# Kernel optimization log

Hardware: AMD Instinct MI355X
Metric: run time of the kernel (lower is better)

## Reference

```python
import jax, jax.numpy as jnp
import numpy as np
from jax import lax

EPS = 1e-5


def maxpool3x3(x):
    # 3x3 max pool, stride 1, pad 1 (NCHW)
    return lax.reduce_window(x, -jnp.inf, lax.max,
                             window_dimensions=(1, 1, 3, 3),
                             window_strides=(1, 1, 1, 1),
                             padding=((0, 0), (0, 0), (1, 1), (1, 1)))


def focus_downsample(x):
    B, C, H, W = x.shape
    pad_h = (3 - H % 3) % 3
    pad_w = (3 - W % 3) % 3
    if pad_h or pad_w:
        x = jnp.pad(x, ((0, 0), (0, 0), (0, pad_h), (0, pad_w)))
    return jnp.concatenate([x[..., i::3, j::3] for i in range(3) for j in range(3)], axis=1)


def batchnorm(x, gamma, beta):
    # training-mode BatchNorm2d: stats over (B,H,W)
    mean = jnp.mean(x, axis=(0, 2, 3), keepdims=True)
    var = jnp.var(x, axis=(0, 2, 3), keepdims=True)
    g = gamma.reshape(1, -1, 1, 1)
    b = beta.reshape(1, -1, 1, 1)
    return (x - mean) * jax.lax.rsqrt(var + EPS) * g + b


def dwconv(x, w, pad_h, pad_w):
    # depthwise conv, w: (C,1,kh,kw)
    return lax.conv_general_dilated(x, w, window_strides=(1, 1),
                                    padding=((pad_h, pad_h), (pad_w, pad_w)),
                                    dimension_numbers=('NCHW', 'OIHW', 'NCHW'),
                                    feature_group_count=x.shape[1])


def h_transform(x):
    B, C, H, W = x.shape
    x = jnp.pad(x, ((0, 0), (0, 0), (0, 0), (0, W)))
    x = x.reshape(B, C, -1)[..., :-W]
    return x.reshape(B, C, H, 2 * W - 1)


def inv_h_transform(x):
    B, C, H, _ = x.shape
    x = x.reshape(B, C, -1)
    x = jnp.pad(x, ((0, 0), (0, 0), (0, H)))
    x = x.reshape(B, C, H, 2 * H)
    return x[..., :H]


def v_transform(x):
    return h_transform(x.transpose(0, 1, 3, 2)).transpose(0, 1, 3, 2)


def inv_v_transform(x):
    return inv_h_transform(x.transpose(0, 1, 3, 2)).transpose(0, 1, 3, 2)


def pixel_shuffle3(x):
    B, C9, h, w = x.shape
    C = C9 // 9
    x = x.reshape(B, C, 3, 3, h, w)
    x = x.transpose(0, 1, 4, 2, 5, 3)  # B,C,h,3,w,3
    return x.reshape(B, C, 3 * h, 3 * w)


def setup_inputs() -> dict:
    key = jax.random.key(0)
    ks = jax.random.split(key, 10)
    C, K = 64, 11
    B, H, W = 16, 144, 144
    s = 0.05
    return {
        'x': jax.random.normal(ks[0], (B, C, H, W), jnp.float32),
        'w_mixer': jax.random.normal(ks[1], (9, C, C), jnp.float32) * s,
        'g_mnorm': jnp.ones((9 * C,), jnp.float32),
        'b_mnorm': jnp.zeros((9 * C,), jnp.float32),
        'w_h1': jax.random.normal(ks[2], (C, 1, K, 3), jnp.float32) * s,
        'w_v1': jax.random.normal(ks[3], (C, 1, 3, K), jnp.float32) * s,
        'w_h2': jax.random.normal(ks[4], (C, 1, K, 3), jnp.float32) * s,
        'w_v2': jax.random.normal(ks[5], (C, 1, 3, K), jnp.float32) * s,
        'g_norm': jnp.ones((C,), jnp.float32),
        'b_norm': jnp.zeros((C,), jnp.float32),
    }


def reference(x, w_mixer, g_mnorm, b_mnorm, w_h1, w_v1, w_h2, w_v2, g_norm, b_norm):
    C = w_h1.shape[0]
    K = w_h1.shape[2]
    pad = K // 2
    H, W = x.shape[-2:]

    x_pool = maxpool3x3(x)
    x_focus = focus_downsample(x_pool)               # (B,9C,H/3,W/3)

    # grouped 1x1 conv, groups=9
    B, _, h, w = x_focus.shape
    xg = x_focus.reshape(B, 9, C, h, w)
    x_mixed = jnp.einsum('goi,bgihw->bgohw', w_mixer, xg).reshape(B, 9 * C, h, w)
    x_mixed = batchnorm(x_mixed, g_mnorm, b_mnorm)

    x_tem, x_key = x_mixed[:, :C], x_mixed[:, C:]

    x_h1 = dwconv(x_tem, w_h1, pad, 1)
    x_w1 = dwconv(x_tem, w_v1, 1, pad)
    x_h2 = inv_h_transform(dwconv(h_transform(x_tem), w_h2, pad, 1))
    x_w2 = inv_v_transform(dwconv(v_transform(x_tem), w_v2, 1, pad))

    att_map = batchnorm(x_h1 + x_w1 + x_h2 + x_w2, g_norm, b_norm)
    final_features = jnp.concatenate([att_map, x_key], axis=1)
    att = pixel_shuffle3(final_features)[..., :H, :W]
    return x * jax.nn.sigmoid(att)
```

## Files before the change

kernel.cpp:

```cpp
#include <hip/hip_runtime.h>
#include <hip/hip_bf16.h>

typedef __hip_bfloat16 bf16;
typedef unsigned short us;
typedef __attribute__((ext_vector_type(8))) short short8;
typedef __attribute__((ext_vector_type(4))) float floatx4;

__device__ __forceinline__ float b2f(bf16 v){ return __bfloat162float(v); }
__device__ __forceinline__ bf16  f2b(float v){ return __float2bfloat16(v); }
__device__ __forceinline__ float ldx(const void* p, size_t i, int isf){
    return isf ? ((const float*)p)[i] : b2f(((const bf16*)p)[i]);
}
__device__ __forceinline__ us bfbits(float v){
    bf16 h = f2b(v); return *(us*)&h;
}
__device__ __forceinline__ float us2f(us u){
    unsigned int w = ((unsigned int)u)<<16; float f; __builtin_memcpy(&f,&w,4); return f;
}

#define BB   16
#define CC   64
#define HH   144
#define WW   144
#define HS   48
#define SP   (HS*HS)
#define NTOT (BB*CC*HH*WW)
#define NCH  36864
#define INV_NCH (1.f/36864.f)

template<int TISF>
__device__ __forceinline__ int isf_of(const int* flag){
    if(TISF >= 0) return TISF;
    return *flag;
}

__global__ void k_sniff(const unsigned int* __restrict__ x, int* __restrict__ flag){
    __shared__ int hit;
    if(threadIdx.x==0) hit = 0;
    __syncthreads();
    int local = 0;
    for(int t=threadIdx.x; t<4096; t+=256){
        unsigned int w = x[t];
        if(((w>>7)&0xFFu)==0xFFu || ((w>>23)&0xFFu)==0xFFu) local = 1;
    }
    if(local) atomicOr(&hit, 1);
    __syncthreads();
    if(threadIdx.x==0) *flag = hit;
}

template<int TISF>
__global__ __launch_bounds__(256) void k_pool3(const void* __restrict__ x,
                                               us* __restrict__ pf,
                                               const int* __restrict__ flag,
                                               float* __restrict__ stats){
    __shared__ float l [18*148];
    __shared__ float hm[18*148];
    int isf = isf_of<TISF>(flag);
    int bid = blockIdx.x;
    int tid = threadIdx.x;
    if(bid==0){
        for(int i=tid; i<1280; i+=256) stats[i] = 0.f;
    }
    int strip = bid % 9;
    int bc = bid / 9;
    int b = bc>>6, c = bc&63;
    int r0 = strip*16;
    size_t base = (size_t)bc*HH*WW;
    for(int t=tid; t<18*18; t+=256){
        int row = t/18, ch = t%18;
        int rr = r0-1+row; int c0 = ch*8;
        float v[8];
        if(rr>=0 && rr<HH){
            if(isf){
                const float* xp = (const float*)x + base + (size_t)rr*WW + c0;
                float4 f0 = *(const float4*)xp;
                float4 f1 = *(const float4*)(xp+4);
                v[0]=f0.x;v[1]=f0.y;v[2]=f0.z;v[3]=f0.w;
                v[4]=f1.x;v[5]=f1.y;v[6]=f1.z;v[7]=f1.w;
            } else {
                const us* xp = (const us*)x + base + (size_t)rr*WW + c0;
                uint4 d = *(const uint4*)xp;
                const us* u = (const us*)&d;
                #pragma unroll
                for(int e=0;e<8;++e) v[e] = us2f(u[e]);
            }
        } else {
            #pragma unroll
            for(int e=0;e<8;++e) v[e] = -INFINITY;
        }
        #pragma unroll
        for(int e=0;e<8;++e) l[row*148 + c0 + e] = v[e];
    }
    __syncthreads();
    for(int t=tid; t<18*144; t+=256){
        int row = t/144, cc = t%144;
        float a = l[row*148+cc];
        float bb = (cc>0)   ? l[row*148+cc-1] : -INFINITY;
        float cv = (cc<143) ? l[row*148+cc+1] : -INFINITY;
        hm[row*148+cc] = fmaxf(a, fmaxf(bb,cv));
    }
    __syncthreads();
    for(int t=tid; t<576; t+=256){
        int row = t/36;
        int gj  = (t/12)%3;
        int xg  = t%12;
        int R = r0+row;
        int gi = R%3, y = R/3;
        union { us u[4]; uint2 v; } pk;
        #pragma unroll
        for(int e=0;e<4;++e){
            int xx = xg*4+e; int C = 3*xx+gj;
            float m = fmaxf(hm[row*148+C],
                      fmaxf(hm[(row+1)*148+C], hm[(row+2)*148+C]));
            pk.u[e] = bfbits(m);
        }
        size_t o = ((((size_t)(b*3+gi)*3+gj)*64 + c)*48 + y)*48 + xg*4;
        *(uint2*)&pf[o] = pk.v;
    }
}

template<int TISF>
__global__ __launch_bounds__(256) void k_mix3(const us* __restrict__ pf,
        const void* __restrict__ wmix, us* __restrict__ mixed,
        float* __restrict__ sum1, float* __restrict__ ss1,
        const int* __restrict__ flag){
    __shared__ __align__(16) us sAll[4096 + 288*64];
    __shared__ float sS[64], sQ[64];
    us* sW = sAll;
    us* sI = sAll + 4096;
    int isf = isf_of<TISF>(flag);
    int bid = blockIdx.x;
    int chunk = bid%8, g = (bid/8)%9, b = bid/72;
    int gi = g/3, gj = g%3;
    int tid = threadIdx.x, lane = tid&63, w = tid>>6;
    {
        int o  = tid>>2;
        int i0 = (tid&3)*16;
        us wb[16];
        if(isf){
            const float* wp = (const float*)wmix + (size_t)g*4096 + (size_t)o*64 + i0;
            #pragma unroll
            for(int e=0;e<16;e+=4){
                float4 f = *(const float4*)(wp+e);
                wb[e]=bfbits(f.x); wb[e+1]=bfbits(f.y);
                wb[e+2]=bfbits(f.z); wb[e+3]=bfbits(f.w);
            }
        } else {
            const us* wp = (const us*)wmix + (size_t)g*4096 + (size_t)o*64 + i0;
            uint4 d0 = *(const uint4*)wp, d1 = *(const uint4*)(wp+8);
            const us* u0 = (const us*)&d0; const us* u1 = (const us*)&d1;
            #pragma unroll
            for(int e=0;e<8;++e){ wb[e]=u0[e]; wb[8+e]=u1[e]; }
        }
        #pragma unroll
        for(int e=0;e<16;++e){
            int i = i0+e;
            sW[o*64 + ((((i>>3)+o)&7)<<3) + (i&7)] = wb[e];
        }
    }
    if(tid<64){ sS[tid]=0.f; sQ[tid]=0.f; }
    {
        int i = lane;
        const us* src = pf + ((((size_t)(b*3+gi)*3+gj)*64 + i)*48 + (size_t)chunk*6)*48;
        for(int vv=w*9; vv<(w+1)*9; ++vv){
            uint4 d = *(const uint4*)(src + vv*8);
            const us* u = (const us*)&d;
            #pragma unroll
            for(int e=0;e<8;++e){
                int s = vv*8+e;
                sI[s*64 + ((((i>>3)+s)&7)<<3) + (i&7)] = u[e];
            }
        }
    }
    __syncthreads();
    int n = lane&15, quad = lane>>4;
    int m = w*16 + n;
    short8 a0 = *(const short8*)&sW[m*64 + (((quad     + m)&7)<<3)];
    short8 a1 = *(const short8*)&sW[m*64 + ((((4+quad) + m)&7)<<3)];
    floatx4 acc[18];
    #pragma unroll
    for(int nt=0; nt<18; ++nt) acc[nt] = (floatx4){0.f,0.f,0.f,0.f};
    #pragma unroll
    for(int nt=0; nt<18; ++nt){
        int site = nt*16 + n;
        short8 b0 = *(const short8*)&sI[site*64 + (((quad     + site)&7)<<3)];
        short8 b1 = *(const short8*)&sI[site*64 + ((((4+quad) + site)&7)<<3)];
        acc[nt] = __builtin_amdgcn_mfma_f32_16x16x32_bf16(a0, b0, acc[nt], 0,0,0);
        acc[nt] = __builtin_amdgcn_mfma_f32_16x16x32_bf16(a1, b1, acc[nt], 0,0,0);
    }
    float s[4] = {0,0,0,0}, q[4] = {0,0,0,0};
    #pragma unroll
    for(int nt=0; nt<18; ++nt){
        #pragma unroll
        for(int r=0;r<4;++r){
            float v = acc[nt][r];
            s[r] += v; q[r] += v*v;
        }
    }
    #pragma unroll
    for(int off=1; off<=8; off<<=1){
        #pragma unroll
        for(int r=0;r<4;++r){
            s[r] += __shfl_xor(s[r], off, 64);
            q[r] += __shfl_xor(q[r], off, 64);
        }
    }
    if(n==0){
        #pragma unroll
        for(int r=0;r<4;++r){
            atomicAdd(&sS[w*16+quad*4+r], s[r]);
            atomicAdd(&sQ[w*16+quad*4+r], q[r]);
        }
    }
    __syncthreads();
    if(tid<64){
        atomicAdd(&sum1[g*64+tid], sS[tid]);
        atomicAdd(&ss1 [g*64+tid], sQ[tid]);
    }
    us* swr = sAll + w*640;
    int o_loc = lane>>2, s8 = (lane&3)*8;
    size_t rowbase = ((size_t)(b*576 + g*64 + w*16))*SP + (size_t)chunk*288;
    #pragma unroll
    for(int mp=0; mp<9; ++mp){
        __builtin_amdgcn_wave_barrier();
        #pragma unroll
        for(int half=0; half<2; ++half){
            int nt = mp*2 + half;
            #pragma unroll
            for(int r=0;r<4;++r)
                swr[(quad*4+r)*40 + half*16 + n] = bfbits(acc[nt][r]);
        }
        __builtin_amdgcn_wave_barrier();
        uint4 vv = *(const uint4*)&swr[o_loc*40 + s8];
        *(uint4*)&mixed[rowbase + (size_t)o_loc*SP + (size_t)(mp*32 + s8)] = vv;
    }
}

template<int TISF>
__global__ __launch_bounds__(256) void k_conv3(const us* __restrict__ mixed,
    const float* __restrict__ sum1, const float* __restrict__ ss1,
    const void* __restrict__ gm, const void* __restrict__ bm,
    const void* __restrict__ wh1, const void* __restrict__ wv1,
    const void* __restrict__ wh2, const void* __restrict__ wv2,
    us* __restrict__ att, float* __restrict__ sum2, float* __restrict__ ss2,
    const int* __restrict__ flag){
    __shared__ float tile[60*60+4];
    __shared__ float w1[33], w2[33], w34[39];
    __shared__ float r1[256], r2[256];
    int isf = isf_of<TISF>(flag);
    int bid = blockIdx.x;
    int b = bid/64, c = bid%64;
    int tid = threadIdx.x;
    for(int t=tid; t<3604; t+=256) tile[t] = 0.f;
    if(tid < 33){
        w1[tid] = ldx(wh1, c*33 + tid, isf);
    } else if(tid < 66){
        w2[tid-33] = ldx(wv1, c*33 + (tid-33), isf);
    } else if(tid < 105){
        int k = tid-66;
        int r = k/3 - 6;
        int vo = k%3 - 1;
        float a = 0.f;
        if(r >= -5 && r <= 5)
            a += ldx(wh2, c*33 + (r+5)*3 + (vo+1), isf);
        int u = vo - r;
        if(u >= -5 && u <= 5)
            a += ldx(wv2, c*33 + (vo+1)*11 + (u+5), isf);
        w34[k] = a;
    }
    __syncthreads();
    float mu   = sum1[c]*INV_NCH;
    float var  = ss1[c]*INV_NCH - mu*mu;
    float is   = rsqrtf(var + 1e-5f)*ldx(gm,c,isf);
    float be   = ldx(bm,c,isf);
    const us* src = mixed + (size_t)(b*576 + c)*SP;
    float w1r[33], w2r[33], w34r[39];
    #pragma unroll
    for(int i=0;i<33;++i) w1r[i] = w1[i];
    #pragma unroll
    for(int i=0;i<33;++i) w2r[i] = w2[i];
    #pragma unroll
    for(int i=0;i<39;++i) w34r[i] = w34[i];
    for(int t=tid; t<288; t+=256){
        int h = t/6, w0 = (t%6)*8;
        uint4 d = *(const uint4*)(src + t*8);
        const us* u = (const us*)&d;
        #pragma unroll
        for(int e=0;e<8;++e)
            tile[(h+6)*60 + (w0+6) + e] = (us2f(u[e]) - mu)*is + be;
    }
    __syncthreads();
    us* out = att + (size_t)(b*64 + c)*SP;
    float sl = 0.f, ql = 0.f;
    #pragma unroll 1
    for(int it=0; it<9; ++it){
        int t = it*256 + tid;
        int hh = t/48 + 6, w = t%48 + 6;
        const float* bp = &tile[hh*60 + w];
        float acc = 0.f;
        #pragma unroll
        for(int r=-1; r<=1; ++r)
            #pragma unroll
            for(int v=-5; v<=5; ++v)
                acc += w2r[(r+1)*11 + (v+5)] * bp[r*60 + v];
        #pragma unroll
        for(int r=-5; r<=5; ++r)
            #pragma unroll
            for(int v=-1; v<=1; ++v)
                acc += w1r[(r+5)*3 + (v+1)] * bp[r*60 + v];
        #pragma unroll
        for(int r=-6; r<=6; ++r)
            #pragma unroll
            for(int v=-1; v<=1; ++v)
                acc += w34r[(r+6)*3 + (v+1)] * bp[r*60 + (v-r)];
        out[t] = bfbits(acc);
        sl += acc; ql += acc*acc;
    }
    r1[tid]=sl; r2[tid]=ql; __syncthreads();
    for(int o=128;o>0;o>>=1){
        if(tid<o){ r1[tid]+=r1[tid+o]; r2[tid]+=r2[tid+o]; }
        __syncthreads();
    }
    if(tid==0){
        atomicAdd(&sum2[c], r1[0]);
        atomicAdd(&ss2 [c], r2[0]);
    }
}

template<int TISF>
__global__ __launch_bounds__(256) void k_final3(const void* __restrict__ x,
    const us* __restrict__ mixed, const us* __restrict__ att,
    const void* __restrict__ gm, const void* __restrict__ bm,
    const void* __restrict__ gn, const void* __restrict__ bnb,
    const float* __restrict__ sum1, const float* __restrict__ ss1,
    const float* __restrict__ sum2, const float* __restrict__ ss2,
    void* __restrict__ out, const int* __restrict__ flag){
    __shared__ __align__(16) us sT[9*1152];
    __shared__ float scs[9], shs[9];
    int isf = isf_of<TISF>(flag);
    int bid = blockIdx.x;
    int half = bid&1, c = (bid>>1)&63, b = bid>>7;
    int yy0 = half*24;
    int tid = threadIdx.x;
    if(tid < 9){
        int f = 9*c + tid;
        float sraw, qraw, gg, bb2;
        if(f < 64){ sraw = sum2[f]; qraw = ss2[f]; gg = ldx(gn,f,isf);  bb2 = ldx(bnb,f,isf); }
        else      { sraw = sum1[f]; qraw = ss1[f]; gg = ldx(gm,f,isf);  bb2 = ldx(bm,f,isf); }
        float mm  = sraw*INV_NCH;
        float ist = rsqrtf(qraw*INV_NCH - mm*mm + 1e-5f);
        float sc = ist*gg;
        scs[tid] = sc;
        shs[tid] = bb2 - mm*sc;
    }
    for(int t=tid; t<9*144; t+=256){
        int j = t/144, qq = t%144;
        int f = 9*c + j;
        const us* srcp = ((f<64) ? att   + (size_t)(b*64 +f)*SP
                                 : mixed + (size_t)(b*576+f)*SP) + yy0*48;
        ((uint4*)&sT[j*1152])[qq] = ((const uint4*)srcp)[qq];
    }
    __syncthreads();
    size_t pbase = (size_t)(b*64+c)*HH*WW;
    for(int t=tid; t<1296; t+=256){
        int Yl = t/18;
        int Xb = (t%18)*8;
        int yyl = Yl/3, r = Yl%3;
        float vo[8];
        #pragma unroll
        for(int k=0;k<8;++k){
            int X = Xb+k;
            int xx = X/3, sph = X%3;
            int j = 3*r + sph;
            float raw = us2f(sT[j*1152 + yyl*48 + xx]);
            float v = raw*scs[j] + shs[j];
            vo[k] = 1.f/(1.f + __expf(-v));
        }
        size_t off = pbase + (size_t)(yy0*3 + Yl)*WW + Xb;
        if(isf){
            const float4* xp = (const float4*)((const float*)x + off);
            float4 x0 = xp[0], x1 = xp[1];
            float4 o0, o1;
            o0.x = x0.x*vo[0]; o0.y = x0.y*vo[1]; o0.z = x0.z*vo[2]; o0.w = x0.w*vo[3];
            o1.x = x1.x*vo[4]; o1.y = x1.y*vo[5]; o1.z = x1.z*vo[6]; o1.w = x1.w*vo[7];
            float4* op = (float4*)((float*)out + off);
            op[0] = o0; op[1] = o1;
        } else {
            uint4 xr = *(const uint4*)((const us*)x + off);
            const us* xu = (const us*)&xr;
            union { us u[8]; uint4 v; } pk;
            #pragma unroll
            for(int k=0;k<8;++k)
                pk.u[k] = bfbits(us2f(xu[k])*vo[k]);
            *(uint4*)((us*)out + off) = pk.v;
        }
    }
}


extern "C" void kernel_launch(void* const* d_in, const int* in_sizes, int n_in,
                              void* d_out, int out_size, void* d_ws, size_t ws_size,
                              hipStream_t stream) {
    (void)n_in; (void)out_size; (void)ws_size;
    const void* x    = d_in[0];
    const void* wmix = d_in[1];
    const void* gm   = d_in[2];
    const void* bm   = d_in[3];
    const void* wh1  = d_in[4];
    const void* wv1  = d_in[5];
    const void* wh2  = d_in[6];
    const void* wv2  = d_in[7];
    const void* gn   = d_in[8];
    const void* bnb  = d_in[9];

    us* pf = (us*)d_out;
    char* ws = (char*)d_ws;
    us*    mixed = (us*)   (ws + 0);
    us*    att   = (us*)   (ws + 42467328);
    float* st1a  = (float*)(ws + 47185920);
    float* st1b  = (float*)(ws + 47188224);
    float* st2a  = (float*)(ws + 47190528);
    float* st2b  = (float*)(ws + 47190784);
    int*   flag  = (int*)  (ws + 47191040);

    int isf;
    if(in_sizes[0] == (int)((long long)NTOT*4)) isf = 1;
    else if(in_sizes[0] == (int)((long long)NTOT*2)) isf = 0;
    else isf = -1;

    if(isf < 0)
        k_sniff<<<1, 256, 0, stream>>>((const unsigned int*)x, flag);

#define LAUNCH_ALL(T)                                                          \
    k_pool3<T><<<BB*CC*9, 256, 0, stream>>>(x, pf, flag, st1a);                \
    k_mix3<T><<<BB*9*8, 256, 0, stream>>>(pf, wmix, mixed, st1a, st1b, flag);  \
    k_conv3<T><<<BB*64, 256, 0, stream>>>(mixed, st1a, st1b, gm, bm,           \
                                          wh1, wv1, wh2, wv2, att,             \
                                          st2a, st2b, flag);                   \
    k_final3<T><<<BB*CC*2, 256, 0, stream>>>(x, mixed, att, gm, bm, gn, bnb,   \
                                             st1a, st1b, st2a, st2b, d_out, flag);

    if(isf == 1)      { LAUNCH_ALL(1)  }
    else if(isf == 0) { LAUNCH_ALL(0)  }
    else              { LAUNCH_ALL(-1) }
#undef LAUNCH_ALL
}
```

Before: 250.9 us.

## Register-block depthwise conv to 3x3 outputs per thread with row reuse

```diff
diff --git a/kernel.cpp b/kernel.cpp
--- a/kernel.cpp
+++ b/kernel.cpp
@@ -16,6 +16,9 @@
 }
 __device__ __forceinline__ float us2f(us u){
     unsigned int w = ((unsigned int)u)<<16; float f; __builtin_memcpy(&f,&w,4); return f;
+}
+__device__ __forceinline__ float uniformf(float v){
+    return __int_as_float(__builtin_amdgcn_readfirstlane(__float_as_int(v)));
 }
 
 #define BB   16
@@ -244,14 +247,14 @@
     const void* __restrict__ wh2, const void* __restrict__ wv2,
     us* __restrict__ att, float* __restrict__ sum2, float* __restrict__ ss2,
     const int* __restrict__ flag){
-    __shared__ float tile[60*60+4];
+    __shared__ float tile[60*60+64];
     __shared__ float w1[33], w2[33], w34[39];
     __shared__ float r1[256], r2[256];
     int isf = isf_of<TISF>(flag);
     int bid = blockIdx.x;
     int b = bid/64, c = bid%64;
     int tid = threadIdx.x;
-    for(int t=tid; t<3604; t+=256) tile[t] = 0.f;
+    for(int t=tid; t<3664; t+=256) tile[t] = 0.f;
     if(tid < 33){
         w1[tid] = ldx(wh1, c*33 + tid, isf);
     } else if(tid < 66){
@@ -276,9 +279,9 @@
     const us* src = mixed + (size_t)(b*576 + c)*SP;
     float w1r[33], w2r[33], w34r[39];
     #pragma unroll
-    for(int i=0;i<33;++i) w1r[i] = w1[i];
-    #pragma unroll
-    for(int i=0;i<33;++i) w2r[i] = w2[i];
+    for(int i=0;i<33;++i) w1r[i] = uniformf(w1[i]);
+    #pragma unroll
+    for(int i=0;i<33;++i) w2r[i] = uniformf(w2[i]);
     #pragma unroll
     for(int i=0;i<39;++i) w34r[i] = w34[i];
     for(int t=tid; t<288; t+=256){
@@ -290,32 +293,68 @@
             tile[(h+6)*60 + (w0+6) + e] = (us2f(u[e]) - mu)*is + be;
     }
     __syncthreads();
+    const int cg = tid & 15, rg = tid >> 4;
+    const int W0 = cg*3, H0 = rg*3;
+    const float* tb = &tile[(H0+6)*60 + (W0+6)];
+    float acc[3][3] = {{0.f,0.f,0.f},{0.f,0.f,0.f},{0.f,0.f,0.f}};
+    #pragma unroll
+    for(int ry=-1; ry<=3; ++ry){
+        float R[13];
+        #pragma unroll
+        for(int k=0;k<13;++k) R[k] = tb[ry*60 + (k-5)];
+        #pragma unroll
+        for(int dy=0; dy<3; ++dy){
+            if(ry-dy < -1 || ry-dy > 1) continue;
+            #pragma unroll
+            for(int dc=0; dc<3; ++dc)
+                #pragma unroll
+                for(int v=-5; v<=5; ++v)
+                    acc[dy][dc] += w2r[(ry-dy+1)*11 + (v+5)] * R[dc+v+5];
+        }
+    }
+    #pragma unroll
+    for(int ry=-5; ry<=7; ++ry){
+        float R[5];
+        #pragma unroll
+        for(int k=0;k<5;++k) R[k] = tb[ry*60 + (k-1)];
+        #pragma unroll
+        for(int dy=0; dy<3; ++dy){
+            if(ry-dy < -5 || ry-dy > 5) continue;
+            #pragma unroll
+            for(int dc=0; dc<3; ++dc)
+                #pragma unroll
+                for(int v=-1; v<=1; ++v)
+                    acc[dy][dc] += w1r[(ry-dy+5)*3 + (v+1)] * R[dc+v+1];
+        }
+    }
+    #pragma unroll
+    for(int ry=-6; ry<=8; ++ry){
+        const int dyLo = (ry-6 > 0) ? ry-6 : 0;
+        const int dyHi = (ry+6 < 2) ? ry+6 : 2;
+        const int jLo  = (dyLo - ry) - 1;
+        float R[7];
+        #pragma unroll
+        for(int k=0;k<7;++k) R[k] = tb[ry*60 + jLo + k];
+        #pragma unroll
+        for(int dy=0; dy<3; ++dy){
+            if(dy < dyLo || dy > dyHi) continue;
+            #pragma unroll
+            for(int dc=0; dc<3; ++dc)
+                #pragma unroll
+                for(int v=-1; v<=1; ++v)
+                    acc[dy][dc] += w34r[(ry-dy+6)*3 + (v+1)] * R[(dy-ry)+dc+v - jLo];
+        }
+    }
     us* out = att + (size_t)(b*64 + c)*SP;
     float sl = 0.f, ql = 0.f;
-    #pragma unroll 1
-    for(int it=0; it<9; ++it){
-        int t = it*256 + tid;
-        int hh = t/48 + 6, w = t%48 + 6;
-        const float* bp = &tile[hh*60 + w];
-        float acc = 0.f;
-        #pragma unroll
-        for(int r=-1; r<=1; ++r)
-            #pragma unroll
-            for(int v=-5; v<=5; ++v)
-                acc += w2r[(r+1)*11 + (v+5)] * bp[r*60 + v];
-        #pragma unroll
-        for(int r=-5; r<=5; ++r)
-            #pragma unroll
-            for(int v=-1; v<=1; ++v)
-                acc += w1r[(r+5)*3 + (v+1)] * bp[r*60 + v];
-        #pragma unroll
-        for(int r=-6; r<=6; ++r)
-            #pragma unroll
-            for(int v=-1; v<=1; ++v)
-                acc += w34r[(r+6)*3 + (v+1)] * bp[r*60 + (v-r)];
-        out[t] = bfbits(acc);
-        sl += acc; ql += acc*acc;
-    }
+    #pragma unroll
+    for(int dy=0; dy<3; ++dy)
+        #pragma unroll
+        for(int dc=0; dc<3; ++dc){
+            float a = acc[dy][dc];
+            out[(H0+dy)*48 + W0+dc] = bfbits(a);
+            sl += a; ql += a*a;
+        }
     r1[tid]=sl; r2[tid]=ql; __syncthreads();
     for(int o=128;o>0;o>>=1){
         if(tid<o){ r1[tid]+=r1[tid+o]; r2[tid]+=r2[tid+o]; }
```

Result: no change. 246.4 us (-1.8%).
